# Performance work log

Hardware: AMD Instinct MI355X
Metric: run time of the kernel (lower is better)

## Reference

```python
import jax, jax.numpy as jnp
import numpy as np

D_STATE = 16
D_CONV = 4


def silu(x):
    return x * jax.nn.sigmoid(x)


def selective_scan(x, dt, A, Bm, Cm, Dp):
    # x, dt: (B,L,P); A: (P,N); Bm, Cm: (B,L,N); Dp: (P,)
    dA = jnp.exp(dt[..., None] * A)                    # (B,L,P,N)
    dBx = (dt * x)[..., None] * Bm[:, :, None, :]      # (B,L,P,N)

    def comb(c1, c2):
        a1, b1 = c1
        a2, b2 = c2
        return a1 * a2, a2 * b1 + b2

    _, h = jax.lax.associative_scan(comb, (dA, dBx), axis=1)
    y = jnp.einsum('blpn,bln->blp', h, Cm) + x * Dp
    return y


def mamba(seq, W_in, conv_w, conv_b, W_x, W_dt, b_dt, A_log, Dp, W_out):
    # seq: (B, L, D_model)
    xz = seq @ W_in.T                                  # (B,L,2P)
    P = xz.shape[-1] // 2
    x, z = xz[..., :P], xz[..., P:]
    # causal depthwise conv over L
    xc = jnp.transpose(x, (0, 2, 1))                   # (B,P,L)
    xc = jax.lax.conv_general_dilated(xc, conv_w[:, None, :], (1,),
                                      [(D_CONV - 1, 0)], feature_group_count=P)
    x = silu(jnp.transpose(xc, (0, 2, 1)) + conv_b)    # (B,L,P)
    proj = x @ W_x.T                                   # (B,L, dt_rank+2N)
    dtr = W_dt.shape[1]
    dt = jax.nn.softplus(proj[..., :dtr] @ W_dt.T + b_dt)
    Bm = proj[..., dtr:dtr + D_STATE]
    Cm = proj[..., dtr + D_STATE:]
    A = -jnp.exp(A_log)
    y = selective_scan(x, dt, A, Bm, Cm, Dp)
    y = y * silu(z)
    return y @ W_out.T                                 # (B,L,D_model)


def oss_forward(x1, x2, W_in, conv_w, conv_b, W_x, W_dt, b_dt, A_log, Dp, W_out):
    B, C, H, W = x1.shape
    L = H * W
    seq_h = jnp.transpose(x1.reshape(B, C, L), (0, 2, 1))                       # (B, H*W, C) row-major
    seq_w = jnp.transpose(jnp.transpose(x1, (0, 1, 3, 2)).reshape(B, C, L), (0, 2, 1))  # column-major

    def run(i, s):
        return mamba(s, W_in[i], conv_w[i], conv_b[i], W_x[i], W_dt[i],
                     b_dt[i], A_log[i], Dp[i], W_out[i])

    y_hf = run(0, seq_h)
    y_hb = jnp.flip(run(1, jnp.flip(seq_h, 1)), 1)
    y_wf = run(2, seq_w)
    y_wb = jnp.flip(run(3, jnp.flip(seq_w, 1)), 1)

    y_h = jnp.transpose((y_hf + y_hb).reshape(B, H, W, C), (0, 3, 1, 2))        # (B,C,H,W)
    y_w = jnp.transpose((y_wf + y_wb).reshape(B, W, H, C), (0, 3, 2, 1))        # (B,C,H,W)
    return y_h + y_w + x2


def setup_inputs() -> dict:
    key = jax.random.key(0)
    ks = jax.random.split(key, 12)
    B, C, H, W = 2, 96, 64, 64
    P = 2 * C            # d_inner = expand * d_model = 192
    N = D_STATE
    dtr = -(-C // 16)    # dt_rank = ceil(C/16) = 6
    s = 0.02
    inp = {
        'x1': jax.random.normal(ks[0], (B, C, H, W), jnp.float32),
        'x2': jax.random.normal(ks[1], (B, C, H, W), jnp.float32),
        'W_in': jax.random.normal(ks[2], (4, 2 * P, C), jnp.float32) * s,
        'conv_w': jax.random.normal(ks[3], (4, P, D_CONV), jnp.float32) * s,
        'conv_b': jnp.zeros((4, P), jnp.float32),
        'W_x': jax.random.normal(ks[4], (4, dtr + 2 * N, P), jnp.float32) * s,
        'W_dt': jax.random.normal(ks[5], (4, P, dtr), jnp.float32) * s,
        'b_dt': jax.random.normal(ks[6], (4, P), jnp.float32) * s,
        'A_log': jnp.log(jnp.tile(jnp.arange(1.0, N + 1.0, dtype=jnp.float32), (4, P, 1))),
        'Dp': jnp.ones((4, P), jnp.float32),
        'W_out': jax.random.normal(ks[7], (4, C, P), jnp.float32) * s,
    }
    return inp


def reference(x1, x2, W_in, conv_w, conv_b, W_x, W_dt, b_dt, A_log, Dp, W_out):
    return oss_forward(x1, x2, W_in, conv_w, conv_b, W_x, W_dt, b_dt, A_log, Dp, W_out)
```

## Files before the change

kernel.cpp:

```cpp
#include <hip/hip_runtime.h>

#define D_DIRS 4
#define BB 2
#define CC 96
#define LL 4096
#define PP 192
#define TWOP 384
#define NN 16
#define DTR 6
#define NPROJ 38
#define PROJW 40
#define NCH 256
#define CLEN 16
#define SEQT 24576
#define LOG2E 1.44269504088896340736f

typedef __bf16 bf16x8 __attribute__((ext_vector_type(8)));
typedef float f32x4 __attribute__((ext_vector_type(4)));

__device__ __forceinline__ float fast_softplus(float v) {
    return fmaxf(v, 0.0f) + __logf(1.0f + __expf(-fabsf(v)));
}

__device__ __constant__ float LOGN[16] = {
    0.0f, 0.6931471806f, 1.0986122887f, 1.3862943611f,
    1.6094379124f, 1.7917594692f, 1.9459101091f, 2.0794415417f,
    2.1972245773f, 2.3025850930f, 2.3978952728f, 2.4849066498f,
    2.5649493575f, 2.6390573296f, 2.7080502011f, 2.7725887222f };

#define POWERS(e1, E)                                                    \
    float E##2 = (e1)*(e1), E##4 = E##2*E##2, E##8 = E##4*E##4;          \
    float E##3 = E##2*(e1), E##5 = E##4*(e1), E##6 = E##4*E##2,          \
          E##7 = E##4*E##3, E##9 = E##8*(e1), E##10 = E##8*E##2,         \
          E##11 = E##8*E##3, E##12 = E##8*E##4, E##13 = E##8*E##5,       \
          E##14 = E##8*E##6, E##15 = E##8*E##7, E##16 = E##8*E##8;

__global__ void k_prep(const float* __restrict__ W_in, const float* __restrict__ W_x,
                       const float* __restrict__ W_out, __bf16* __restrict__ wbin,
                       __bf16* __restrict__ wbx, __bf16* __restrict__ wbout)
{
    int i = blockIdx.x * 256 + threadIdx.x;
    const int n0 = 4 * 384 * 104, n1 = 4 * 48 * 200, n2 = 4 * 96 * 200;
    if (i < n0) {
        int c = i % 104, jd = i / 104;
        wbin[i] = (c < 96) ? (__bf16)W_in[jd * 96 + c] : (__bf16)0.0f;
    } else if (i < n0 + n1) {
        int k = i - n0;
        int c = k % 200, jd = k / 200;
        int d = jd / 48, j = jd - d * 48;
        float v = (j < 38 && c < 192) ? W_x[(d * 38 + j) * 192 + c] : 0.0f;
        wbx[k] = (__bf16)v;
    } else if (i < n0 + n1 + n2) {
        int k = i - n0 - n1;
        int c = k % 200, jd = k / 200;
        float v = (c < 192) ? W_out[jd * 192 + c] : 0.0f;
        wbout[k] = (__bf16)v;
    }
}

__global__ __launch_bounds__(256) void k_img(
    const float* __restrict__ x1, __bf16* __restrict__ imgH, __bf16* __restrict__ imgW)
{
    __shared__ float t[96 * 65];
    const int b = blockIdx.y;
    const int lt = blockIdx.x;
    const int tid = threadIdx.x;
    for (int i = tid; i < 96 * 64; i += 256) {
        int c = i >> 6, lw = i & 63;
        t[c * 65 + lw] = x1[((b * 96 + c) << 12) + (lt << 6) + lw];
    }
    __syncthreads();
    for (int i = tid; i < 64 * 12; i += 256) {
        int lw = i / 12, q = i - lw * 12;
        union { __bf16 h[8]; uint4 u; } pk;
#pragma unroll
        for (int j = 0; j < 8; ++j) pk.h[j] = (__bf16)t[(q * 8 + j) * 65 + lw];
        ((uint4*)(imgH + (long)((b << 12) + (lt << 6) + lw) * 104))[q] = pk.u;
        ((uint4*)(imgW + (long)((b << 12) + (lw << 6) + lt) * 104))[q] = pk.u;
    }
}

__global__ __launch_bounds__(256) void k_gemm_in(
    const __bf16* __restrict__ imgH, const __bf16* __restrict__ imgW,
    const __bf16* __restrict__ wbin, float* __restrict__ xz_x, __bf16* __restrict__ zb)
{
    __shared__ __align__(16) __bf16 As[64 * 104];
    __shared__ __align__(16) __bf16 Bs[64 * 104];
    const int db = blockIdx.y;
    const int d = db >> 1, b = db & 1;
    const int t0 = blockIdx.x * 64;
    const int tid = threadIdx.x;
    const __bf16* img = (d < 2 ? imgH : imgW) + (long)b * (LL * 104);

    {
        uint4* adst = (uint4*)As;
        for (int i = tid; i < 832; i += 256) {
            int r = i / 13, q = i - r * 13;
            int l = (d & 1) ? (LL - 1 - (t0 + r)) : (t0 + r);
            adst[i] = ((const uint4*)(img + (long)l * 104))[q];
        }
    }

    const int lane = tid & 63;
    const int w = tid >> 6;
    const int wm = (w >> 1) * 32, wn = (w & 1) * 32;
    const int lr = lane & 15, lk = (lane >> 4) * 8;
    const int orow = (lane >> 4) * 4;

    for (int j0 = 0; j0 < TWOP; j0 += 64) {
        __syncthreads();
        {
            const uint4* bsrc = (const uint4*)(wbin + (long)(d * TWOP + j0) * 104);
            uint4* bdst = (uint4*)Bs;
            for (int i = tid; i < 832; i += 256) bdst[i] = bsrc[i];
        }
        __syncthreads();

        f32x4 acc[2][2] = {{{0.f,0.f,0.f,0.f},{0.f,0.f,0.f,0.f}},
                           {{0.f,0.f,0.f,0.f},{0.f,0.f,0.f,0.f}}};
#pragma unroll
        for (int ks = 0; ks < 96; ks += 32) {
            bf16x8 a0 = *(const bf16x8*)&As[(wm + lr) * 104 + ks + lk];
            bf16x8 a1 = *(const bf16x8*)&As[(wm + 16 + lr) * 104 + ks + lk];
            bf16x8 b0 = *(const bf16x8*)&Bs[(wn + lr) * 104 + ks + lk];
            bf16x8 b1 = *(const bf16x8*)&Bs[(wn + 16 + lr) * 104 + ks + lk];
            acc[0][0] = __builtin_amdgcn_mfma_f32_16x16x32_bf16(a0, b0, acc[0][0], 0, 0, 0);
            acc[0][1] = __builtin_amdgcn_mfma_f32_16x16x32_bf16(a0, b1, acc[0][1], 0, 0, 0);
            acc[1][0] = __builtin_amdgcn_mfma_f32_16x16x32_bf16(a1, b0, acc[1][0], 0, 0, 0);
            acc[1][1] = __builtin_amdgcn_mfma_f32_16x16x32_bf16(a1, b1, acc[1][1], 0, 0, 0);
        }
#pragma unroll
        for (int mi = 0; mi < 2; ++mi)
#pragma unroll
            for (int ni = 0; ni < 2; ++ni) {
                long mbase = (long)(db * LL + t0 + wm + mi * 16 + orow);
                int jcol = j0 + wn + ni * 16 + lr;
                if (j0 < PP) {
#pragma unroll
                    for (int r = 0; r < 4; ++r) xz_x[(mbase + r) * PP + jcol] = acc[mi][ni][r];
                } else {
#pragma unroll
                    for (int r = 0; r < 4; ++r) zb[(mbase + r) * PP + jcol - PP] = (__bf16)acc[mi][ni][r];
                }
            }
    }
}

__global__ __launch_bounds__(192) void k_conv(
    const float* __restrict__ xz_x, const float* __restrict__ conv_w,
    const float* __restrict__ conv_b, __bf16* __restrict__ xb16)
{
    __shared__ float xs[67 * 192];
    const int db = blockIdx.y;
    const int t0 = blockIdx.x * 64;
    const int d = db >> 1;
    const int m0 = db * LL + t0;
    const int tid = threadIdx.x;

    const float4* src = (const float4*)(xz_x + ((long)m0 - 3) * PP);
    for (int i = tid; i < 67 * 48; i += 192) {
        float4 v;
        if (t0 == 0 && i < 144) v = make_float4(0.f, 0.f, 0.f, 0.f);
        else v = src[i];
        ((float4*)xs)[i] = v;
    }

    const int p = tid;
    const float* wp = conv_w + (d * PP + p) * 4;
    float w0 = wp[0], w1 = wp[1], w2 = wp[2], w3 = wp[3];
    float bias = conv_b[d * PP + p];
    __syncthreads();

    for (int t = 0; t < 64; ++t) {
        float acc = bias + w0 * xs[t * PP + p] + w1 * xs[(t + 1) * PP + p]
                         + w2 * xs[(t + 2) * PP + p] + w3 * xs[(t + 3) * PP + p];
        float s = acc / (1.0f + __expf(-acc));
        xb16[(long)(m0 + t) * 200 + p] = (__bf16)s;
    }
}

__global__ __launch_bounds__(256) void k_gemm_proj(
    const __bf16* __restrict__ xb16, const __bf16* __restrict__ wbx, float* __restrict__ proj)
{
    __shared__ __align__(16) __bf16 As[64 * 200];
    __shared__ __align__(16) __bf16 Bs[48 * 200];
    const int m0 = blockIdx.x * 64;
    const int d = m0 >> 13;
    const int tid = threadIdx.x;

    for (int i = tid; i < 1600; i += 256) {
        int r = i / 25, q = i - r * 25;
        ((uint4*)As)[i] = ((const uint4*)(xb16 + (long)(m0 + r) * 200))[q];
    }
    {
        const uint4* bsrc = (const uint4*)(wbx + (long)d * 48 * 200);
        uint4* bdst = (uint4*)Bs;
        for (int i = tid; i < 1200; i += 256) bdst[i] = bsrc[i];
    }
    __syncthreads();

    const int lane = tid & 63;
    const int w = tid >> 6;
    const int lr = lane & 15, lk = (lane >> 4) * 8;
    const int orow = (lane >> 4) * 4;

    f32x4 acc[3] = {{0.f,0.f,0.f,0.f},{0.f,0.f,0.f,0.f},{0.f,0.f,0.f,0.f}};
#pragma unroll
    for (int ks = 0; ks < 192; ks += 32) {
        bf16x8 a = *(const bf16x8*)&As[(w * 16 + lr) * 200 + ks + lk];
#pragma unroll
        for (int ni = 0; ni < 3; ++ni) {
            bf16x8 bfr = *(const bf16x8*)&Bs[(ni * 16 + lr) * 200 + ks + lk];
            acc[ni] = __builtin_amdgcn_mfma_f32_16x16x32_bf16(a, bfr, acc[ni], 0, 0, 0);
        }
    }
#pragma unroll
    for (int ni = 0; ni < 3; ++ni) {
        int j = ni * 16 + lr;
        if (j < NPROJ) {
            int col = (j < 6) ? j : j + 2;
#pragma unroll
            for (int r = 0; r < 4; ++r) {
                int m = m0 + w * 16 + orow + r;
                proj[(long)m * PROJW + col] = acc[ni][r];
            }
        }
    }
}

__global__ __launch_bounds__(256) void k_gemm_out(
    const __bf16* __restrict__ ysb, const __bf16* __restrict__ wbout, float* __restrict__ yo)
{
    __shared__ __align__(16) __bf16 As[64 * 200];
    __shared__ __align__(16) __bf16 Bs[96 * 200];
    const int m0 = blockIdx.x * 64;
    const int d = m0 >> 13;
    const int tid = threadIdx.x;

    for (int i = tid; i < 1600; i += 256) {
        int r = i / 25, q = i - r * 25;
        ((uint4*)As)[i] = ((const uint4*)(ysb + (long)(m0 + r) * 200))[q];
    }
    {
        const uint4* bsrc = (const uint4*)(wbout + (long)d * 96 * 200);
        uint4* bdst = (uint4*)Bs;
        for (int i = tid; i < 2400; i += 256) bdst[i] = bsrc[i];
    }
    __syncthreads();

    const int lane = tid & 63;
    const int w = tid >> 6;
    const int wm = (w >> 1) * 32, wn = (w & 1) * 48;
    const int lr = lane & 15, lk = (lane >> 4) * 8;
    const int orow = (lane >> 4) * 4;

    f32x4 acc[2][3] = {};
#pragma unroll
    for (int ks = 0; ks < 192; ks += 32) {
        bf16x8 a0 = *(const bf16x8*)&As[(wm + lr) * 200 + ks + lk];
        bf16x8 a1 = *(const bf16x8*)&As[(wm + 16 + lr) * 200 + ks + lk];
#pragma unroll
        for (int ni = 0; ni < 3; ++ni) {
            bf16x8 bfr = *(const bf16x8*)&Bs[(wn + ni * 16 + lr) * 200 + ks + lk];
            acc[0][ni] = __builtin_amdgcn_mfma_f32_16x16x32_bf16(a0, bfr, acc[0][ni], 0, 0, 0);
            acc[1][ni] = __builtin_amdgcn_mfma_f32_16x16x32_bf16(a1, bfr, acc[1][ni], 0, 0, 0);
        }
    }
#pragma unroll
    for (int mi = 0; mi < 2; ++mi)
#pragma unroll
        for (int ni = 0; ni < 3; ++ni) {
#pragma unroll
            for (int r = 0; r < 4; ++r) {
                int m = m0 + wm + mi * 16 + orow + r;
                yo[(long)m * CC + wn + ni * 16 + lr] = acc[mi][ni][r];
            }
        }
}

__global__ __launch_bounds__(192) void k_pass1(
    const __bf16* __restrict__ xb16, const float* __restrict__ proj,
    const float* __restrict__ A_log, const float* __restrict__ W_dt,
    const float* __restrict__ b_dt,
    float* __restrict__ cb_pa, float* __restrict__ cb_h)
{
    const int p = threadIdx.x;
    const int chunk = blockIdx.x;
    const int db = blockIdx.y;
    const int d = db >> 1;
    const int m0 = db * LL + chunk * CLEN;

    bool fastA = true;
    float A2[16];
    {
        const float* al = A_log + (d * PP + p) * NN;
#pragma unroll
        for (int n = 0; n < 16; ++n) {
            float av = al[n];
            fastA = fastA && (fabsf(av - LOGN[n]) < 1e-4f);
            A2[n] = av;
        }
    }
    float w[6];
    const float* wd = W_dt + (d * PP + p) * DTR;
#pragma unroll
    for (int r = 0; r < 6; ++r) w[r] = wd[r];
    const float bdt = b_dt[d * PP + p];
    float h[16];
#pragma unroll
    for (int n = 0; n < 16; ++n) h[n] = 0.f;
    float sdt = 0.f;

    const float* prow = proj + (long)m0 * PROJW;
    const __bf16* xrow = xb16 + (long)m0 * 200 + p;

    if (fastA) {
#pragma unroll
        for (int s = 0; s < CLEN; ++s) {
            const float* row = prow + s * PROJW;
            float4 d0 = *(const float4*)(row);
            float4 d1 = *(const float4*)(row + 4);
            float v = bdt + d0.x*w[0] + d0.y*w[1] + d0.z*w[2] + d0.w*w[3] + d1.x*w[4] + d1.y*w[5];
            float dtv = fast_softplus(v);
            sdt += dtv;
            float dtx = dtv * (float)xrow[s * 200];
            float e1 = exp2f(-LOG2E * dtv);
            POWERS(e1, e)
            const float4* B4 = (const float4*)(row + 8);
            float4 B0 = B4[0], B1 = B4[1], B2v = B4[2], B3 = B4[3];
            h[0]  = e1 *h[0]  + dtx*B0.x;  h[1]  = e2 *h[1]  + dtx*B0.y;
            h[2]  = e3 *h[2]  + dtx*B0.z;  h[3]  = e4 *h[3]  + dtx*B0.w;
            h[4]  = e5 *h[4]  + dtx*B1.x;  h[5]  = e6 *h[5]  + dtx*B1.y;
            h[6]  = e7 *h[6]  + dtx*B1.z;  h[7]  = e8 *h[7]  + dtx*B1.w;
            h[8]  = e9 *h[8]  + dtx*B2v.x; h[9]  = e10*h[9]  + dtx*B2v.y;
            h[10] = e11*h[10] + dtx*B2v.z; h[11] = e12*h[11] + dtx*B2v.w;
            h[12] = e13*h[12] + dtx*B3.x;  h[13] = e14*h[13] + dtx*B3.y;
            h[14] = e15*h[14] + dtx*B3.z;  h[15] = e16*h[15] + dtx*B3.w;
        }
        const long cbase = (long)chunk * SEQT + db * PP + p;
        float pe1 = exp2f(-LOG2E * sdt);
        POWERS(pe1, pe)
        float pa[16] = {pe1,pe2,pe3,pe4,pe5,pe6,pe7,pe8,pe9,pe10,pe11,pe12,pe13,pe14,pe15,pe16};
#pragma unroll
        for (int n = 0; n < 16; ++n) {
            cb_pa[cbase + n * 1536] = pa[n];
            cb_h [cbase + n * 1536] = h[n];
        }
    } else {
#pragma unroll
        for (int n = 0; n < 16; ++n) A2[n] = -__expf(A2[n]) * LOG2E;
        for (int s = 0; s < CLEN; ++s) {
            const float* row = prow + s * PROJW;
            float4 d0 = *(const float4*)(row);
            float4 d1 = *(const float4*)(row + 4);
            float v = bdt + d0.x*w[0] + d0.y*w[1] + d0.z*w[2] + d0.w*w[3] + d1.x*w[4] + d1.y*w[5];
            float dtv = fast_softplus(v);
            sdt += dtv;
            float dtx = dtv * (float)xrow[s * 200];
            const float* B = row + 8;
#pragma unroll
            for (int n = 0; n < 16; ++n)
                h[n] = exp2f(dtv * A2[n]) * h[n] + dtx * B[n];
        }
        const long cbase = (long)chunk * SEQT + db * PP + p;
#pragma unroll
        for (int n = 0; n < 16; ++n) {
            cb_pa[cbase + n * 1536] = exp2f(A2[n] * sdt);
            cb_h [cbase + n * 1536] = h[n];
        }
    }
}

__global__ void k_chunkscan(const float* __restrict__ cb_pa, float* __restrict__ cb_h)
{
    int j = blockIdx.x * 256 + threadIdx.x;
    float run = 0.0f;
    for (int c = 0; c < NCH; c += 8) {
        float pa[8], hh[8];
#pragma unroll
        for (int i = 0; i < 8; ++i) {
            long o = (long)(c + i) * SEQT + j;
            pa[i] = cb_pa[o]; hh[i] = cb_h[o];
        }
#pragma unroll
        for (int i = 0; i < 8; ++i) {
            cb_h[(long)(c + i) * SEQT + j] = run;
            run = pa[i] * run + hh[i];
        }
    }
}

__global__ __launch_bounds__(192) void k_pass2(
    const __bf16* __restrict__ xb16, const float* __restrict__ proj,
    const float* __restrict__ A_log, const float* __restrict__ W_dt,
    const float* __restrict__ b_dt, const float* __restrict__ Dp,
    const __bf16* __restrict__ zb, const float* __restrict__ cb_h,
    __bf16* __restrict__ ysb)
{
    const int p = threadIdx.x;
    const int chunk = blockIdx.x;
    const int db = blockIdx.y;
    const int d = db >> 1;
    const int m0 = db * LL + chunk * CLEN;

    bool fastA = true;
    float A2[16];
    {
        const float* al = A_log + (d * PP + p) * NN;
#pragma unroll
        for (int n = 0; n < 16; ++n) {
            float av = al[n];
            fastA = fastA && (fabsf(av - LOGN[n]) < 1e-4f);
            A2[n] = av;
        }
    }
    float w[6];
    const float* wd = W_dt + (d * PP + p) * DTR;
#pragma unroll
    for (int r = 0; r < 6; ++r) w[r] = wd[r];
    const float bdt = b_dt[d * PP + p];
    const float Dv = Dp[d * PP + p];

    float h[16];
    const long cbase = (long)chunk * SEQT + db * PP + p;
#pragma unroll
    for (int n = 0; n < 16; ++n) h[n] = cb_h[cbase + n * 1536];

    const float* prow = proj + (long)m0 * PROJW;
    const __bf16* xrow = xb16 + (long)m0 * 200 + p;
    const __bf16* zrow = zb + (long)m0 * PP + p;
    __bf16* yrow = ysb + (long)m0 * 200 + p;

    if (fastA) {
#pragma unroll
        for (int s = 0; s < CLEN; ++s) {
            const float* row = prow + s * PROJW;
            float4 d0 = *(const float4*)(row);
            float4 d1 = *(const float4*)(row + 4);
            float v = bdt + d0.x*w[0] + d0.y*w[1] + d0.z*w[2] + d0.w*w[3] + d1.x*w[4] + d1.y*w[5];
            float dtv = fast_softplus(v);
            float xvv = (float)xrow[s * 200];
            float dtx = dtv * xvv;
            float e1 = exp2f(-LOG2E * dtv);
            POWERS(e1, e)
            const float4* B4 = (const float4*)(row + 8);
            const float4* C4 = (const float4*)(row + 24);
            float4 B0 = B4[0], B1 = B4[1], B2v = B4[2], B3 = B4[3];
            float4 C0 = C4[0], C1 = C4[1], C2v = C4[2], C3 = C4[3];
            float y = 0.f;
            h[0]  = e1 *h[0]  + dtx*B0.x;  y += h[0] *C0.x;
            h[1]  = e2 *h[1]  + dtx*B0.y;  y += h[1] *C0.y;
            h[2]  = e3 *h[2]  + dtx*B0.z;  y += h[2] *C0.z;
            h[3]  = e4 *h[3]  + dtx*B0.w;  y += h[3] *C0.w;
            h[4]  = e5 *h[4]  + dtx*B1.x;  y += h[4] *C1.x;
            h[5]  = e6 *h[5]  + dtx*B1.y;  y += h[5] *C1.y;
            h[6]  = e7 *h[6]  + dtx*B1.z;  y += h[6] *C1.z;
            h[7]  = e8 *h[7]  + dtx*B1.w;  y += h[7] *C1.w;
            h[8]  = e9 *h[8]  + dtx*B2v.x; y += h[8] *C2v.x;
            h[9]  = e10*h[9]  + dtx*B2v.y; y += h[9] *C2v.y;
            h[10] = e11*h[10] + dtx*B2v.z; y += h[10]*C2v.z;
            h[11] = e12*h[11] + dtx*B2v.w; y += h[11]*C2v.w;
            h[12] = e13*h[12] + dtx*B3.x;  y += h[12]*C3.x;
            h[13] = e14*h[13] + dtx*B3.y;  y += h[13]*C3.y;
            h[14] = e15*h[14] + dtx*B3.z;  y += h[14]*C3.z;
            h[15] = e16*h[15] + dtx*B3.w;  y += h[15]*C3.w;
            float zvv = (float)zrow[s * PP];
            yrow[s * 200] = (__bf16)((y + xvv * Dv) * (zvv / (1.0f + __expf(-zvv))));
        }
    } else {
#pragma unroll
        for (int n = 0; n < 16; ++n) A2[n] = -__expf(A2[n]) * LOG2E;
        for (int s = 0; s < CLEN; ++s) {
            const float* row = prow + s * PROJW;
            float4 d0 = *(const float4*)(row);
            float4 d1 = *(const float4*)(row + 4);
            float v = bdt + d0.x*w[0] + d0.y*w[1] + d0.z*w[2] + d0.w*w[3] + d1.x*w[4] + d1.y*w[5];
            float dtv = fast_softplus(v);
            float xvv = (float)xrow[s * 200];
            float dtx = dtv * xvv;
            const float* B = row + 8;
            const float* C = row + 24;
            float y = 0.f;
#pragma unroll
            for (int n = 0; n < 16; ++n) {
                h[n] = exp2f(dtv * A2[n]) * h[n] + dtx * B[n];
                y += h[n] * C[n];
            }
            float zvv = (float)zrow[s * PP];
            yrow[s * 200] = (__bf16)((y + xvv * Dv) * (zvv / (1.0f + __expf(-zvv))));
        }
    }
}

__global__ void k_final(const float* __restrict__ x2, const float* __restrict__ yo,
                        float* __restrict__ out)
{
    int idx = blockIdx.x * blockDim.x + threadIdx.x;
    const int total = BB * CC * LL;
    for (; idx < total; idx += gridDim.x * blockDim.x) {
        int w = idx & 63;
        int h = (idx >> 6) & 63;
        int c = (idx >> 12) % CC;
        int b = idx / (CC * LL);
        int lh = (h << 6) | w;
        int lw = (w << 6) | h;
        long m0 = (long)(0 * BB + b) * LL + lh;
        long m1 = (long)(1 * BB + b) * LL + (LL - 1 - lh);
        long m2 = (long)(2 * BB + b) * LL + lw;
        long m3 = (long)(3 * BB + b) * LL + (LL - 1 - lw);
        out[idx] = x2[idx] + yo[m0 * CC + c] + yo[m1 * CC + c] + yo[m2 * CC + c] + yo[m3 * CC + c];
    }
}

extern "C" void kernel_launch(void* const* d_in, const int* in_sizes, int n_in,
                              void* d_out, int out_size, void* d_ws, size_t ws_size,
                              hipStream_t stream)
{
    const float* x1     = (const float*)d_in[0];
    const float* x2     = (const float*)d_in[1];
    const float* W_in   = (const float*)d_in[2];
    const float* conv_w = (const float*)d_in[3];
    const float* conv_b = (const float*)d_in[4];
    const float* W_x    = (const float*)d_in[5];
    const float* W_dt   = (const float*)d_in[6];
    const float* b_dt   = (const float*)d_in[7];
    const float* A_log  = (const float*)d_in[8];
    const float* Dp     = (const float*)d_in[9];
    const float* W_out  = (const float*)d_in[10];
    float* out = (float*)d_out;
    float* ws  = (float*)d_ws;

    float*  xz_x  = ws;
    __bf16* zb    = (__bf16*)(ws + 6291456);
    __bf16* xb16  = (__bf16*)(ws + 9437184);
    float*  proj  = ws + 12713984;
    float*  cb_pa = ws + 14024704;
    float*  cb_h  = ws + 20316160;
    __bf16* imgH  = (__bf16*)(ws + 26607616);
    __bf16* imgW  = (__bf16*)(ws + 27033600);
    __bf16* wbin  = (__bf16*)(ws + 27459584);
    __bf16* wbx   = (__bf16*)(ws + 27539456);
    __bf16* wbout = (__bf16*)(ws + 27558656);
    __bf16* ysb = (__bf16*)xz_x;
    float*  yo  = cb_pa;

    k_prep<<<dim3(1074), 256, 0, stream>>>(W_in, W_x, W_out, wbin, wbx, wbout);
    k_img<<<dim3(64, 2), 256, 0, stream>>>(x1, imgH, imgW);
    k_gemm_in<<<dim3(64, 8), 256, 0, stream>>>(imgH, imgW, wbin, xz_x, zb);
    k_conv<<<dim3(64, 8), 192, 0, stream>>>(xz_x, conv_w, conv_b, xb16);
    k_gemm_proj<<<dim3(512), 256, 0, stream>>>(xb16, wbx, proj);
    k_pass1<<<dim3(NCH, 8), 192, 0, stream>>>(xb16, proj, A_log, W_dt, b_dt, cb_pa, cb_h);
    k_chunkscan<<<dim3(SEQT / 256), 256, 0, stream>>>(cb_pa, cb_h);
    k_pass2<<<dim3(NCH, 8), 192, 0, stream>>>(xb16, proj, A_log, W_dt, b_dt, Dp, zb, cb_h, ysb);
    k_gemm_out<<<dim3(512), 256, 0, stream>>>(ysb, wbout, yo);
    k_final<<<dim3(3072), 256, 0, stream>>>(x2, yo, out);
}
```

Baseline: 145.5 us.

## Fuse conv into projection GEMM and merge weight prep with image transpose

Merges the weight-conversion and image-transpose kernels into one launch split by block index, and fuses the causal depthwise conv+SiLU into the x-projection GEMM kernel. The conv result now goes straight into shared memory as the GEMM A tile, which removes one launch and a global reload of xb16. Three threads' worth of waves do the conv while the fourth wave loads weights. The conv now reads xz_x directly from global memory with a sliding register window instead of staging it in shared memory, which adds strided global loads per thread.

Result: faster. 131.8 us (-9.4%).

```diff
diff --git a/kernel.cpp b/kernel.cpp
--- a/kernel.cpp
+++ b/kernel.cpp
@@ -35,48 +35,49 @@
           E##11 = E##8*E##3, E##12 = E##8*E##4, E##13 = E##8*E##5,       \
           E##14 = E##8*E##6, E##15 = E##8*E##7, E##16 = E##8*E##8;
 
-__global__ void k_prep(const float* __restrict__ W_in, const float* __restrict__ W_x,
-                       const float* __restrict__ W_out, __bf16* __restrict__ wbin,
-                       __bf16* __restrict__ wbx, __bf16* __restrict__ wbout)
-{
-    int i = blockIdx.x * 256 + threadIdx.x;
-    const int n0 = 4 * 384 * 104, n1 = 4 * 48 * 200, n2 = 4 * 96 * 200;
-    if (i < n0) {
-        int c = i % 104, jd = i / 104;
-        wbin[i] = (c < 96) ? (__bf16)W_in[jd * 96 + c] : (__bf16)0.0f;
-    } else if (i < n0 + n1) {
-        int k = i - n0;
-        int c = k % 200, jd = k / 200;
-        int d = jd / 48, j = jd - d * 48;
-        float v = (j < 38 && c < 192) ? W_x[(d * 38 + j) * 192 + c] : 0.0f;
-        wbx[k] = (__bf16)v;
-    } else if (i < n0 + n1 + n2) {
-        int k = i - n0 - n1;
-        int c = k % 200, jd = k / 200;
-        float v = (c < 192) ? W_out[jd * 192 + c] : 0.0f;
-        wbout[k] = (__bf16)v;
-    }
-}
-
-__global__ __launch_bounds__(256) void k_img(
-    const float* __restrict__ x1, __bf16* __restrict__ imgH, __bf16* __restrict__ imgW)
+__global__ __launch_bounds__(256) void k_setup(
+    const float* __restrict__ W_in, const float* __restrict__ W_x,
+    const float* __restrict__ W_out, const float* __restrict__ x1,
+    __bf16* __restrict__ wbin, __bf16* __restrict__ wbx, __bf16* __restrict__ wbout,
+    __bf16* __restrict__ imgH, __bf16* __restrict__ imgW)
 {
     __shared__ float t[96 * 65];
-    const int b = blockIdx.y;
-    const int lt = blockIdx.x;
     const int tid = threadIdx.x;
-    for (int i = tid; i < 96 * 64; i += 256) {
-        int c = i >> 6, lw = i & 63;
-        t[c * 65 + lw] = x1[((b * 96 + c) << 12) + (lt << 6) + lw];
-    }
-    __syncthreads();
-    for (int i = tid; i < 64 * 12; i += 256) {
-        int lw = i / 12, q = i - lw * 12;
-        union { __bf16 h[8]; uint4 u; } pk;
-#pragma unroll
-        for (int j = 0; j < 8; ++j) pk.h[j] = (__bf16)t[(q * 8 + j) * 65 + lw];
-        ((uint4*)(imgH + (long)((b << 12) + (lt << 6) + lw) * 104))[q] = pk.u;
-        ((uint4*)(imgW + (long)((b << 12) + (lw << 6) + lt) * 104))[q] = pk.u;
+    if (blockIdx.x < 1074) {
+        int i = blockIdx.x * 256 + tid;
+        const int n0 = 4 * 384 * 104, n1 = 4 * 48 * 200, n2 = 4 * 96 * 200;
+        if (i < n0) {
+            int c = i % 104, jd = i / 104;
+            wbin[i] = (c < 96) ? (__bf16)W_in[jd * 96 + c] : (__bf16)0.0f;
+        } else if (i < n0 + n1) {
+            int k = i - n0;
+            int c = k % 200, jd = k / 200;
+            int d = jd / 48, j = jd - d * 48;
+            float v = (j < 38 && c < 192) ? W_x[(d * 38 + j) * 192 + c] : 0.0f;
+            wbx[k] = (__bf16)v;
+        } else if (i < n0 + n1 + n2) {
+            int k = i - n0 - n1;
+            int c = k % 200, jd = k / 200;
+            float v = (c < 192) ? W_out[jd * 192 + c] : 0.0f;
+            wbout[k] = (__bf16)v;
+        }
+    } else {
+        const int bx = blockIdx.x - 1074;
+        const int b = bx >> 6;
+        const int lt = bx & 63;
+        for (int i = tid; i < 96 * 64; i += 256) {
+            int c = i >> 6, lw = i & 63;
+            t[c * 65 + lw] = x1[((b * 96 + c) << 12) + (lt << 6) + lw];
+        }
+        __syncthreads();
+        for (int i = tid; i < 64 * 12; i += 256) {
+            int lw = i / 12, q = i - lw * 12;
+            union { __bf16 h[8]; uint4 u; } pk;
+#pragma unroll
+            for (int j = 0; j < 8; ++j) pk.h[j] = (__bf16)t[(q * 8 + j) * 65 + lw];
+            ((uint4*)(imgH + (long)((b << 12) + (lt << 6) + lw) * 104))[q] = pk.u;
+            ((uint4*)(imgW + (long)((b << 12) + (lw << 6) + lt) * 104))[q] = pk.u;
+        }
     }
 }
 
@@ -146,56 +147,42 @@
     }
 }
 
-__global__ __launch_bounds__(192) void k_conv(
+__global__ __launch_bounds__(256) void k_convproj(
     const float* __restrict__ xz_x, const float* __restrict__ conv_w,
-    const float* __restrict__ conv_b, __bf16* __restrict__ xb16)
-{
-    __shared__ float xs[67 * 192];
+    const float* __restrict__ conv_b, const __bf16* __restrict__ wbx,
+    __bf16* __restrict__ xb16, float* __restrict__ proj)
+{
+    __shared__ __align__(16) __bf16 As[64 * 200];
+    __shared__ __align__(16) __bf16 Bs[48 * 200];
     const int db = blockIdx.y;
+    const int d = db >> 1;
     const int t0 = blockIdx.x * 64;
-    const int d = db >> 1;
     const int m0 = db * LL + t0;
     const int tid = threadIdx.x;
 
-    const float4* src = (const float4*)(xz_x + ((long)m0 - 3) * PP);
-    for (int i = tid; i < 67 * 48; i += 192) {
-        float4 v;
-        if (t0 == 0 && i < 144) v = make_float4(0.f, 0.f, 0.f, 0.f);
-        else v = src[i];
-        ((float4*)xs)[i] = v;
-    }
-
-    const int p = tid;
-    const float* wp = conv_w + (d * PP + p) * 4;
-    float w0 = wp[0], w1 = wp[1], w2 = wp[2], w3 = wp[3];
-    float bias = conv_b[d * PP + p];
-    __syncthreads();
-
-    for (int t = 0; t < 64; ++t) {
-        float acc = bias + w0 * xs[t * PP + p] + w1 * xs[(t + 1) * PP + p]
-                         + w2 * xs[(t + 2) * PP + p] + w3 * xs[(t + 3) * PP + p];
-        float s = acc / (1.0f + __expf(-acc));
-        xb16[(long)(m0 + t) * 200 + p] = (__bf16)s;
-    }
-}
-
-__global__ __launch_bounds__(256) void k_gemm_proj(
-    const __bf16* __restrict__ xb16, const __bf16* __restrict__ wbx, float* __restrict__ proj)
-{
-    __shared__ __align__(16) __bf16 As[64 * 200];
-    __shared__ __align__(16) __bf16 Bs[48 * 200];
-    const int m0 = blockIdx.x * 64;
-    const int d = m0 >> 13;
-    const int tid = threadIdx.x;
-
-    for (int i = tid; i < 1600; i += 256) {
-        int r = i / 25, q = i - r * 25;
-        ((uint4*)As)[i] = ((const uint4*)(xb16 + (long)(m0 + r) * 200))[q];
-    }
-    {
+    if (tid < 192) {
+        const int p = tid;
+        const float* wp = conv_w + (d * PP + p) * 4;
+        float w0 = wp[0], w1 = wp[1], w2 = wp[2], w3 = wp[3];
+        float bias = conv_b[d * PP + p];
+        const float* xcol = xz_x + (long)m0 * PP + p;
+        float x0, x1, x2;
+        if (t0 == 0) { x0 = 0.f; x1 = 0.f; x2 = 0.f; }
+        else { x0 = xcol[-3 * PP]; x1 = xcol[-2 * PP]; x2 = xcol[-PP]; }
+#pragma unroll 8
+        for (int t = 0; t < 64; ++t) {
+            float x3 = xcol[t * PP];
+            float acc = bias + w0 * x0 + w1 * x1 + w2 * x2 + w3 * x3;
+            float s = acc / (1.0f + __expf(-acc));
+            __bf16 sb = (__bf16)s;
+            As[t * 200 + p] = sb;
+            xb16[(long)(m0 + t) * 200 + p] = sb;
+            x0 = x1; x1 = x2; x2 = x3;
+        }
+    } else {
         const uint4* bsrc = (const uint4*)(wbx + (long)d * 48 * 200);
         uint4* bdst = (uint4*)Bs;
-        for (int i = tid; i < 1200; i += 256) bdst[i] = bsrc[i];
+        for (int i = tid - 192; i < 1200; i += 64) bdst[i] = bsrc[i];
     }
     __syncthreads();
 
@@ -544,11 +531,9 @@
     __bf16* ysb = (__bf16*)xz_x;
     float*  yo  = cb_pa;
 
-    k_prep<<<dim3(1074), 256, 0, stream>>>(W_in, W_x, W_out, wbin, wbx, wbout);
-    k_img<<<dim3(64, 2), 256, 0, stream>>>(x1, imgH, imgW);
+    k_setup<<<dim3(1202), 256, 0, stream>>>(W_in, W_x, W_out, x1, wbin, wbx, wbout, imgH, imgW);
     k_gemm_in<<<dim3(64, 8), 256, 0, stream>>>(imgH, imgW, wbin, xz_x, zb);
-    k_conv<<<dim3(64, 8), 192, 0, stream>>>(xz_x, conv_w, conv_b, xb16);
-    k_gemm_proj<<<dim3(512), 256, 0, stream>>>(xb16, wbx, proj);
+    k_convproj<<<dim3(64, 8), 256, 0, stream>>>(xz_x, conv_w, conv_b, wbx, xb16, proj);
     k_pass1<<<dim3(NCH, 8), 192, 0, stream>>>(xb16, proj, A_log, W_dt, b_dt, cb_pa, cb_h);
     k_chunkscan<<<dim3(SEQT / 256), 256, 0, stream>>>(cb_pa, cb_h);
     k_pass2<<<dim3(NCH, 8), 192, 0, stream>>>(xb16, proj, A_log, W_dt, b_dt, Dp, zb, cb_h, ysb);
```
